# Kernel tuning notes

Measured on AMD Instinct MI355X. Metric: run time of the kernel, lower is better.

Reference implementation:

```python
import jax, jax.numpy as jnp
import numpy as np

EMBED_DIM = 512
NUM_HEADS = 16
WIN = (8, 8)
N_TOK = WIN[0] * WIN[1]           # 64 tokens per window
HEAD_DIM = EMBED_DIM // NUM_HEADS  # 32
SCALE = HEAD_DIM ** -0.5
B_WIN = 1024                       # batch * num_windows
NUM_WINDOWS = 256                  # windows per image -> batch images = 4


def _relative_bias_index(window_size):
    wh, ww = window_size
    coords = np.stack(np.meshgrid(np.arange(wh), np.arange(ww), indexing='ij'))  # (2, wh, ww)
    flat = coords.reshape(2, -1)                                   # (2, N)
    rel = (flat[:, :, None] - flat[:, None, :]).transpose(1, 2, 0)  # (N, N, 2)
    rel[:, :, 0] += wh - 1
    rel[:, :, 1] += ww - 1
    rel[:, :, 0] *= 2 * ww - 1
    return rel.sum(-1)  # (N, N) int


def setup_inputs() -> dict:
    key = jax.random.key(0)
    ks = jax.random.split(key, 6)
    x = jax.random.normal(ks[0], (B_WIN, N_TOK, EMBED_DIM), dtype=jnp.float32)
    attention_mask = jax.random.normal(ks[1], (NUM_WINDOWS, N_TOK, N_TOK), dtype=jnp.float32)
    qkv_w = jax.random.normal(ks[2], (EMBED_DIM, 3 * EMBED_DIM), dtype=jnp.float32) * 0.02
    qkv_b = jnp.zeros((3 * EMBED_DIM,), dtype=jnp.float32)
    proj_w = jax.random.normal(ks[3], (EMBED_DIM, EMBED_DIM), dtype=jnp.float32) * 0.02
    proj_b = jnp.zeros((EMBED_DIM,), dtype=jnp.float32)
    n_bias = (2 * WIN[0] - 1) * (2 * WIN[1] - 1)  # 225
    bias_table = jax.random.normal(ks[4], (n_bias, NUM_HEADS), dtype=jnp.float32) * 0.02
    rel_index = jnp.asarray(_relative_bias_index(WIN), dtype=jnp.int32)  # (N, N)
    return {"x": x, "attention_mask": attention_mask, "qkv_w": qkv_w, "qkv_b": qkv_b,
            "proj_w": proj_w, "proj_b": proj_b, "bias_table": bias_table, "rel_index": rel_index}


def reference(x, attention_mask, qkv_w, qkv_b, proj_w, proj_b, bias_table, rel_index):
    B, N, C = x.shape
    nw = attention_mask.shape[0]
    bimg = B // nw
    qkv = x @ qkv_w + qkv_b                              # (B, N, 3C)
    # original rearrange 'b n (h d c) -> d b n h c' groups last dim as (heads, 3, head_dim)
    qkv = qkv.reshape(B, N, NUM_HEADS, 3, HEAD_DIM)
    q, k, v = qkv[..., 0, :], qkv[..., 1, :], qkv[..., 2, :]  # each (B, N, H, hd)
    attn = jnp.einsum('bqhd,bkhd->bhqk', q, k) * SCALE        # (B, H, N, N)
    bias = bias_table[rel_index].transpose(2, 0, 1)           # (H, N, N)
    attn = attn + bias[None]
    attn = attn.reshape(bimg, nw, NUM_HEADS, N, N) + attention_mask[None, :, None]
    attn = jax.nn.softmax(attn, axis=-1).reshape(B, NUM_HEADS, N, N)
    out = jnp.einsum('bhqk,bkhd->bqhd', attn, v).reshape(B, N, C)
    return out @ proj_w + proj_b
```

## Files before the change

### kernel.cpp

```cpp
#include <hip/hip_runtime.h>
#include <hip/hip_bf16.h>


typedef unsigned short u16;
typedef __bf16 bx8 __attribute__((ext_vector_type(8)));
typedef float f4_t __attribute__((ext_vector_type(4)));

#define QKV_ELEMS 33554432ull
#define SCALE 0.17677669529663687f

static __device__ __forceinline__ u16 f2b(float f) {
    return __builtin_bit_cast(u16, (__bf16)f);
}

typedef const unsigned int __attribute__((address_space(1)))* gas_t;
typedef unsigned int __attribute__((address_space(3)))* las_t;
static __device__ __forceinline__ void glds16(const void* g, void* l) {
    __builtin_amdgcn_global_load_lds((gas_t)g, (las_t)l, 16, 0, 0);
}

__global__ __launch_bounds__(256) void prep_k(
    const float* __restrict__ X, u16* __restrict__ Xb,
    const float* __restrict__ qkv_w, u16* __restrict__ Wt1,
    const float* __restrict__ proj_w, u16* __restrict__ Wt2,
    const float* __restrict__ bias_t, const int* __restrict__ rel,
    float* __restrict__ biasf) {
    const int b = blockIdx.x;
    if (b < 16384) {
        size_t i = ((size_t)b * 256 + threadIdx.x) * 8;
        float4 v0 = *(const float4*)(X + i);
        float4 v1 = *(const float4*)(X + i + 4);
        ushort4 p0, p1;
        p0.x = f2b(v0.x); p0.y = f2b(v0.y); p0.z = f2b(v0.z); p0.w = f2b(v0.w);
        p1.x = f2b(v1.x); p1.y = f2b(v1.y); p1.z = f2b(v1.z); p1.w = f2b(v1.w);
        *(ushort4*)(Xb + i) = p0;
        *(ushort4*)(Xb + i + 4) = p1;
    } else if (b < 16384 + 3072) {
        int idx = (b - 16384) * 256 + threadIdx.x;
        int n = idx >> 9, k = idx & 511;
        Wt1[idx] = f2b(qkv_w[(size_t)k * 1536 + n]);
    } else if (b < 16384 + 4096) {
        int idx = (b - 16384 - 3072) * 256 + threadIdx.x;
        int n = idx >> 9, k = idx & 511;
        Wt2[idx] = f2b(proj_w[(size_t)k * 512 + n]);
    } else {
        int idx = (b - 16384 - 4096) * 256 + threadIdx.x;
        int h = idx >> 12, rc = idx & 4095;
        biasf[idx] = bias_t[rel[rc] * 16 + h];
    }
}


#define MF1(av, bv, mt, nt)                                                   \
    acc[mt][nt] = __builtin_amdgcn_mfma_f32_16x16x32_bf16(av, bv,             \
                                                          acc[mt][nt], 0, 0, 0);
#define MF4(av, mt, B)                                                        \
    MF1(av, B[0], mt, 0) MF1(av, B[1], mt, 1)                                 \
    MF1(av, B[2], mt, 2) MF1(av, B[3], mt, 3)

#define PH_EVEN(T, DOST, BCUR)                                                \
    {                                                                         \
        asm volatile("s_barrier" ::: "memory");                               \
        const char* aT = ldsA + ((T) & 3) * 16384 + wm * 8192 + foff;         \
        aHi[0] = *(const bx8*)(aT + 4096);                                    \
        aHi[1] = *(const bx8*)(aT + 5120);                                    \
        aHi[2] = *(const bx8*)(aT + 6144);                                    \
        aHi[3] = *(const bx8*)(aT + 7168);                                    \
        if (DOST) STAGE_A((T) + 3);                                           \
        asm volatile("s_waitcnt lgkmcnt(4)" ::: "memory");                    \
        __builtin_amdgcn_sched_barrier(0);                                    \
        __builtin_amdgcn_s_setprio(1);                                        \
        MF4(aLo[0], 0, BCUR) MF4(aLo[1], 1, BCUR)                             \
        MF4(aLo[2], 2, BCUR) MF4(aLo[3], 3, BCUR)                             \
        __builtin_amdgcn_s_setprio(0);                                        \
    }

#define PH_ODD(T, DOST, VMC, DORD, BCUR, BNXT)                                \
    {                                                                         \
        if ((VMC) == 6) asm volatile("s_waitcnt vmcnt(6)" ::: "memory");      \
        else if ((VMC) == 4) asm volatile("s_waitcnt vmcnt(4)" ::: "memory"); \
        else if ((VMC) == 0) asm volatile("s_waitcnt vmcnt(0)" ::: "memory"); \
        asm volatile("s_barrier" ::: "memory");                               \
        if (DORD) {                                                           \
            const char* aN = ldsA + (((T) + 1) & 3) * 16384 + wm * 8192 + foff;\
            const char* bN = ldsB + (((T) + 1) & 3) * 16384 + wn * 4096 + foff;\
            BNXT[0] = *(const bx8*)(bN);                                      \
            BNXT[1] = *(const bx8*)(bN + 1024);                               \
            BNXT[2] = *(const bx8*)(bN + 2048);                               \
            BNXT[3] = *(const bx8*)(bN + 3072);                               \
            aLo[0] = *(const bx8*)(aN);                                       \
            aLo[1] = *(const bx8*)(aN + 1024);                                \
            aLo[2] = *(const bx8*)(aN + 2048);                                \
            aLo[3] = *(const bx8*)(aN + 3072);                                \
        }                                                                     \
        if (DOST) STAGE_B((T) + 3);                                           \
        if (DORD) asm volatile("s_waitcnt lgkmcnt(8)" ::: "memory");          \
        else      asm volatile("s_waitcnt lgkmcnt(0)" ::: "memory");          \
        __builtin_amdgcn_sched_barrier(0);                                    \
        __builtin_amdgcn_s_setprio(1);                                        \
        MF4(aHi[0], 4, BCUR) MF4(aHi[1], 5, BCUR)                             \
        MF4(aHi[2], 6, BCUR) MF4(aHi[3], 7, BCUR)                             \
        __builtin_amdgcn_s_setprio(0);                                        \
    }

template <int MODE>
__global__ __launch_bounds__(512, 2) void gemm256_k(
    const u16* __restrict__ A, const u16* __restrict__ Bt,
    const float* __restrict__ bias, void* __restrict__ Out) {
    extern __shared__ __align__(16) char smem[];
    const int tid = threadIdx.x;
    const int wave = tid >> 6, lane = tid & 63;
    const int l16 = lane & 15, quad = lane >> 4;
    const int wm = wave >> 2, wn = wave & 3;

    const int NT_COL = (MODE == 0) ? 6 : 2;
    const int NWG = (MODE == 0) ? 1536 : 512;
    const int bid = blockIdx.x;
    const int swz = (bid & 7) * (NWG >> 3) + (bid >> 3);
    const int m0 = (swz / NT_COL) << 8;
    const int n0 = (swz % NT_COL) << 8;

    char* const ldsA = smem;
    char* const ldsB = smem + 65536;

    const int lr = lane >> 2, lc = lane & 3;
    const int swzc = (lc ^ ((lr >> 1) & 3)) * 8;
    const int stoff = wave * 1024;

    const u16* Asrc0;
    const u16* Asrc1;
    if (MODE == 0) {
        const int r0 = m0 + wave * 16 + lr;
        Asrc0 = A + (size_t)r0 * 512 + swzc;
        Asrc1 = Asrc0 + (size_t)128 * 512;
    } else {
        const int r0 = m0 + wave * 16 + lr, r1 = r0 + 128;
        Asrc0 = A + (size_t)(r0 >> 6) * 2048 + (r0 & 63) * 32 + swzc;
        Asrc1 = A + (size_t)(r1 >> 6) * 2048 + (r1 & 63) * 32 + swzc;
    }
    const u16* Bsrc0 = Bt + (size_t)(n0 + wave * 16 + lr) * 512 + swzc;
    const u16* Bsrc1 = Bsrc0 + (size_t)128 * 512;

    auto STAGE_A = [&](int T) {
        char* d = ldsA + (T & 3) * 16384 + stoff;
        if (MODE == 0) {
            glds16(Asrc0 + T * 32, d);
            glds16(Asrc1 + T * 32, d + 8192);
        } else {
            glds16(Asrc0 + (size_t)T * 2097152, d);
            glds16(Asrc1 + (size_t)T * 2097152, d + 8192);
        }
    };
    auto STAGE_B = [&](int T) {
        char* d = ldsB + (T & 3) * 16384 + stoff;
        glds16(Bsrc0 + T * 32, d);
        glds16(Bsrc1 + T * 32, d + 8192);
    };

    const int foff = l16 * 64 + ((quad ^ ((l16 >> 1) & 3)) * 16);

    f4_t acc[8][4];
#pragma unroll
    for (int i = 0; i < 8; ++i)
#pragma unroll
        for (int j = 0; j < 4; ++j) acc[i][j] = (f4_t){0.f, 0.f, 0.f, 0.f};

    bx8 aLo[4], aHi[4], bA[4], bB[4];

    STAGE_A(0); STAGE_B(0); STAGE_A(1); STAGE_B(1); STAGE_A(2); STAGE_B(2);
    asm volatile("s_waitcnt vmcnt(8)" ::: "memory");
    asm volatile("s_barrier" ::: "memory");
    {
        const char* aT = ldsA + wm * 8192 + foff;
        const char* bT = ldsB + wn * 4096 + foff;
        bA[0] = *(const bx8*)(bT);
        bA[1] = *(const bx8*)(bT + 1024);
        bA[2] = *(const bx8*)(bT + 2048);
        bA[3] = *(const bx8*)(bT + 3072);
        aLo[0] = *(const bx8*)(aT);
        aLo[1] = *(const bx8*)(aT + 1024);
        aLo[2] = *(const bx8*)(aT + 2048);
        aLo[3] = *(const bx8*)(aT + 3072);
    }

    PH_EVEN(0, 1, bA)  PH_ODD(0, 1, 6, 1, bA, bB)
    PH_EVEN(1, 1, bB)  PH_ODD(1, 1, 6, 1, bB, bA)
    PH_EVEN(2, 1, bA)  PH_ODD(2, 1, 6, 1, bA, bB)
    PH_EVEN(3, 1, bB)  PH_ODD(3, 1, 6, 1, bB, bA)
    PH_EVEN(4, 1, bA)  PH_ODD(4, 1, 6, 1, bA, bB)
    PH_EVEN(5, 1, bB)  PH_ODD(5, 1, 6, 1, bB, bA)
    PH_EVEN(6, 1, bA)  PH_ODD(6, 1, 6, 1, bA, bB)
    PH_EVEN(7, 1, bB)  PH_ODD(7, 1, 6, 1, bB, bA)
    PH_EVEN(8, 1, bA)  PH_ODD(8, 1, 6, 1, bA, bB)
    PH_EVEN(9, 1, bB)  PH_ODD(9, 1, 6, 1, bB, bA)
    PH_EVEN(10, 1, bA) PH_ODD(10, 1, 6, 1, bA, bB)
    PH_EVEN(11, 1, bB) PH_ODD(11, 1, 6, 1, bB, bA)
    PH_EVEN(12, 1, bA) PH_ODD(12, 1, 6, 1, bA, bB)
    PH_EVEN(13, 0, bB) PH_ODD(13, 0, 4, 1, bB, bA)
    PH_EVEN(14, 0, bA) PH_ODD(14, 0, 0, 1, bA, bB)
    PH_EVEN(15, 0, bB) PH_ODD(15, 0, -1, 0, bB, bA)

    __syncthreads();

    float bv[4];
#pragma unroll
    for (int nt = 0; nt < 4; ++nt) bv[nt] = bias[n0 + wn * 64 + nt * 16 + l16];

    if (MODE == 0) {
        u16* c_s = (u16*)smem;
        u16* qkvp = (u16*)Out;
        const int cg = n0 + wave * 32;
        const int hh = cg / 96;
        const int which = (cg - hh * 96) >> 5;
        u16* plane = qkvp + (size_t)which * QKV_ELEMS + (size_t)hh * 2048;
#pragma unroll
        for (int p = 0; p < 2; ++p) {
            if (wm == p) {
#pragma unroll
                for (int mt = 0; mt < 8; ++mt)
#pragma unroll
                    for (int nt = 0; nt < 4; ++nt)
#pragma unroll
                        for (int i = 0; i < 4; ++i)
                            c_s[(mt * 16 + quad * 4 + i) * 264 +
                                wn * 64 + nt * 16 + l16] =
                                f2b(acc[mt][nt][i] + bv[nt]);
            }
            __syncthreads();
#pragma unroll
            for (int j = 0; j < 8; ++j) {
                int row = j * 16 + (lane >> 2);
                int gm = m0 + p * 128 + row;
                int w_win = gm >> 6, tok = gm & 63;
                uint4 v = *(const uint4*)&c_s[row * 264 + wave * 32 +
                                              (lane & 3) * 8];
                *(uint4*)(plane + (size_t)w_win * 32768 + tok * 32 +
                          (lane & 3) * 8) = v;
            }
            __syncthreads();
        }
    } else {
        float* c_sf = (float*)smem;
        float* Of = (float*)Out;
#pragma unroll
        for (int p = 0; p < 4; ++p) {
            if (wm == (p >> 1)) {
                const int mtb = (p & 1) * 4;
#pragma unroll
                for (int mt2 = 0; mt2 < 4; ++mt2)
#pragma unroll
                    for (int nt = 0; nt < 4; ++nt)
#pragma unroll
                        for (int i = 0; i < 4; ++i)
                            c_sf[(mt2 * 16 + quad * 4 + i) * 264 +
                                 wn * 64 + nt * 16 + l16] =
                                acc[mtb + mt2][nt][i] + bv[nt];
            }
            __syncthreads();
#pragma unroll
            for (int j = 0; j < 8; ++j) {
                int flat = tid + 512 * j;
                int r = flat >> 6, c4 = (flat & 63) * 4;
                float4 v = *(const float4*)&c_sf[r * 264 + c4];
                *(float4*)&Of[(size_t)(m0 + p * 64 + r) * 512 + n0 + c4] = v;
            }
            __syncthreads();
        }
    }
}

__global__ __launch_bounds__(256, 4) void attn_k(
    const u16* __restrict__ qkv, const float* __restrict__ mask,
    const float* __restrict__ biasf, u16* __restrict__ attn_out) {
    const int bx = blockIdx.x;
    const int w = bx >> 4, h = bx & 15;
    const int wmk = w & 255;
    const int tid = threadIdx.x;
    const int wave = tid >> 6, lane = tid & 63;
    const int quad = lane >> 4, l16 = lane & 15;

    __shared__ alignas(16) u16 q_s[64 * 40];
    __shared__ alignas(16) u16 k_s[64 * 40];
    __shared__ alignas(16) u16 vT[32 * 72];
    __shared__ alignas(16) float s_s[64 * 65];
    __shared__ alignas(16) u16 p_s[64 * 72];

    const size_t base = (size_t)((w << 4) + h) * 2048;
    {
        int tok = tid >> 2, d0 = (tid & 3) * 8;
        uint4 qv = *(const uint4*)(qkv + base + tid * 8);
        *(uint4*)&q_s[tok * 40 + d0] = qv;
        uint4 kv = *(const uint4*)(qkv + QKV_ELEMS + base + tid * 8);
        *(uint4*)&k_s[tok * 40 + d0] = kv;
        uint4 vv = *(const uint4*)(qkv + 2 * QKV_ELEMS + base + tid * 8);
        const u16* pv = (const u16*)&vv;
#pragma unroll
        for (int j = 0; j < 8; ++j) vT[(d0 + j) * 72 + tok] = pv[j];
    }
    __syncthreads();

    {
        bx8 a = *(const bx8*)&q_s[(wave * 16 + l16) * 40 + quad * 8];
#pragma unroll
        for (int nt = 0; nt < 4; ++nt) {
            bx8 b = *(const bx8*)&k_s[(nt * 16 + l16) * 40 + quad * 8];
            f4_t acc = (f4_t){0.f, 0.f, 0.f, 0.f};
            acc = __builtin_amdgcn_mfma_f32_16x16x32_bf16(a, b, acc, 0, 0, 0);
#pragma unroll
            for (int i = 0; i < 4; ++i) {
                int r = wave * 16 + quad * 4 + i;
                int c = nt * 16 + l16;
                float s = acc[i] * SCALE + biasf[(h << 12) + (r << 6) + c] +
                          mask[((size_t)wmk * 64 + r) * 64 + c];
                s_s[r * 65 + c] = s;
            }
        }
    }
    __syncthreads();

    {
        int row = tid >> 2, j = (tid & 3) * 16;
        float mx = -1e30f;
#pragma unroll
        for (int cc = 0; cc < 16; ++cc) mx = fmaxf(mx, s_s[row * 65 + j + cc]);
        mx = fmaxf(mx, __shfl_xor(mx, 1));
        mx = fmaxf(mx, __shfl_xor(mx, 2));
        float e[16], sum = 0.f;
#pragma unroll
        for (int cc = 0; cc < 16; ++cc) {
            e[cc] = __expf(s_s[row * 65 + j + cc] - mx);
            sum += e[cc];
        }
        sum += __shfl_xor(sum, 1);
        sum += __shfl_xor(sum, 2);
        float inv = 1.f / sum;
#pragma unroll
        for (int cc = 0; cc < 16; ++cc) p_s[row * 72 + j + cc] = f2b(e[cc] * inv);
    }
    __syncthreads();

    {
        u16* os = (u16*)s_s;
#pragma unroll
        for (int nt = 0; nt < 2; ++nt) {
            f4_t acc = (f4_t){0.f, 0.f, 0.f, 0.f};
#pragma unroll
            for (int ks = 0; ks < 2; ++ks) {
                bx8 a = *(const bx8*)&p_s[(wave * 16 + l16) * 72 + ks * 32 + quad * 8];
                bx8 b = *(const bx8*)&vT[(nt * 16 + l16) * 72 + ks * 32 + quad * 8];
                acc = __builtin_amdgcn_mfma_f32_16x16x32_bf16(a, b, acc, 0, 0, 0);
            }
#pragma unroll
            for (int i = 0; i < 4; ++i)
                os[(wave * 16 + quad * 4 + i) * 40 + nt * 16 + l16] =
                    f2b(acc[i]);
        }
        __syncthreads();
        int tok = tid >> 2, d8 = (tid & 3) * 8;
        uint4 v = *(const uint4*)&os[tok * 40 + d8];
        *(uint4*)(attn_out + ((((size_t)h << 10) + w) << 11) + tid * 8) = v;
    }
}

extern "C" void kernel_launch(void* const* d_in, const int* in_sizes, int n_in,
                              void* d_out, int out_size, void* d_ws,
                              size_t ws_size, hipStream_t stream) {
    const float* x      = (const float*)d_in[0];
    const float* mask   = (const float*)d_in[1];
    const float* qkv_w  = (const float*)d_in[2];
    const float* qkv_b  = (const float*)d_in[3];
    const float* proj_w = (const float*)d_in[4];
    const float* proj_b = (const float*)d_in[5];
    const float* bias_t = (const float*)d_in[6];
    const int*   rel    = (const int*)d_in[7];
    float* out = (float*)d_out;

    char* ws = (char*)d_ws;
    u16* Wt1 = (u16*)ws;      ws += (size_t)1536 * 512 * 2;
    u16* Wt2 = (u16*)ws;      ws += (size_t)512 * 512 * 2;
    float* biasf = (float*)ws; ws += (size_t)16 * 64 * 64 * 4;
    u16* qkv = (u16*)ws;      ws += 3 * QKV_ELEMS * 2;
    u16* attn = (u16*)ws;     ws += QKV_ELEMS * 2;
    u16* xb = attn;

    prep_k<<<20736, 256, 0, stream>>>(x, xb, qkv_w, Wt1, proj_w, Wt2,
                                      bias_t, rel, biasf);
    gemm256_k<0><<<1536, 512, 131072, stream>>>(xb, Wt1, qkv_b, qkv);
    attn_k<<<16384, 256, 0, stream>>>(qkv, mask, biasf, attn);
    gemm256_k<1><<<512, 512, 131072, stream>>>(attn, Wt2, proj_b, out);
}
```

Measured before the change: 484.9 us.

## Restructure GEMM main loop to K=64 tiles with double buffering

The GEMM kernel's mainloop moves from sixteen K=32 steps over a 4-stage LDS ring to eight K=64 steps with two LDS buffers of 64KB each. The LDS swizzle and staging layout change to match. This halves the number of barriers and lets each stage issue larger batches of async loads. The cost is a shallower prefetch depth (one tile ahead, with a full vmcnt(0) wait before each barrier), which can expose global-load latency.

```diff
diff --git a/kernel.cpp b/kernel.cpp
--- a/kernel.cpp
+++ b/kernel.cpp
@@ -51,60 +51,75 @@
 }
 
 
-#define MF1(av, bv, mt, nt)                                                   \
-    acc[mt][nt] = __builtin_amdgcn_mfma_f32_16x16x32_bf16(av, bv,             \
-                                                          acc[mt][nt], 0, 0, 0);
-#define MF4(av, mt, B)                                                        \
-    MF1(av, B[0], mt, 0) MF1(av, B[1], mt, 1)                                 \
-    MF1(av, B[2], mt, 2) MF1(av, B[3], mt, 3)
-
-#define PH_EVEN(T, DOST, BCUR)                                                \
+#define MF1(av, bv, mi, nt)                                                   \
+    acc[mi][nt] = __builtin_amdgcn_mfma_f32_16x16x32_bf16(av, bv,             \
+                                                          acc[mi][nt], 0, 0, 0);
+#define MF16(A4, mb, B4)                                                      \
+    MF1(A4[0], B4[0], (mb)+0, 0) MF1(A4[0], B4[1], (mb)+0, 1)                 \
+    MF1(A4[0], B4[2], (mb)+0, 2) MF1(A4[0], B4[3], (mb)+0, 3)                 \
+    MF1(A4[1], B4[0], (mb)+1, 0) MF1(A4[1], B4[1], (mb)+1, 1)                 \
+    MF1(A4[1], B4[2], (mb)+1, 2) MF1(A4[1], B4[3], (mb)+1, 3)                 \
+    MF1(A4[2], B4[0], (mb)+2, 0) MF1(A4[2], B4[1], (mb)+2, 1)                 \
+    MF1(A4[2], B4[2], (mb)+2, 2) MF1(A4[2], B4[3], (mb)+2, 3)                 \
+    MF1(A4[3], B4[0], (mb)+3, 0) MF1(A4[3], B4[1], (mb)+3, 1)                 \
+    MF1(A4[3], B4[2], (mb)+3, 2) MF1(A4[3], B4[3], (mb)+3, 3)
+
+#define ARD4(dst, sb, mh, kh)                                                 \
+    dst[0] = *(const bx8*)((sb) + awoff + ((mh)*4+0)*2048 + aoffk##kh);       \
+    dst[1] = *(const bx8*)((sb) + awoff + ((mh)*4+1)*2048 + aoffk##kh);       \
+    dst[2] = *(const bx8*)((sb) + awoff + ((mh)*4+2)*2048 + aoffk##kh);       \
+    dst[3] = *(const bx8*)((sb) + awoff + ((mh)*4+3)*2048 + aoffk##kh);
+#define BRD4(dst, sb, kh)                                                     \
+    dst[0] = *(const bx8*)((sb) + bwoff + 0*2048 + aoffk##kh);                \
+    dst[1] = *(const bx8*)((sb) + bwoff + 1*2048 + aoffk##kh);                \
+    dst[2] = *(const bx8*)((sb) + bwoff + 2*2048 + aoffk##kh);                \
+    dst[3] = *(const bx8*)((sb) + bwoff + 3*2048 + aoffk##kh);
+
+#define TILE64(T, DOST, LAST)                                                 \
     {                                                                         \
-        asm volatile("s_barrier" ::: "memory");                               \
-        const char* aT = ldsA + ((T) & 3) * 16384 + wm * 8192 + foff;         \
-        aHi[0] = *(const bx8*)(aT + 4096);                                    \
-        aHi[1] = *(const bx8*)(aT + 5120);                                    \
-        aHi[2] = *(const bx8*)(aT + 6144);                                    \
-        aHi[3] = *(const bx8*)(aT + 7168);                                    \
-        if (DOST) STAGE_A((T) + 3);                                           \
+        const char* sb = smem + ((T) & 1) * 65536;                            \
+        const char* sn = smem + (((T) + 1) & 1) * 65536;                      \
+                          \
+        ARD4(aN, sb, 1, 0)                                                    \
+        if (DOST) STAGE((T) + 1);                                             \
         asm volatile("s_waitcnt lgkmcnt(4)" ::: "memory");                    \
         __builtin_amdgcn_sched_barrier(0);                                    \
         __builtin_amdgcn_s_setprio(1);                                        \
-        MF4(aLo[0], 0, BCUR) MF4(aLo[1], 1, BCUR)                             \
-        MF4(aLo[2], 2, BCUR) MF4(aLo[3], 3, BCUR)                             \
+        MF16(aC, 0, b0)                                                       \
         __builtin_amdgcn_s_setprio(0);                                        \
-    }
-
-#define PH_ODD(T, DOST, VMC, DORD, BCUR, BNXT)                                \
-    {                                                                         \
-        if ((VMC) == 6) asm volatile("s_waitcnt vmcnt(6)" ::: "memory");      \
-        else if ((VMC) == 4) asm volatile("s_waitcnt vmcnt(4)" ::: "memory"); \
-        else if ((VMC) == 0) asm volatile("s_waitcnt vmcnt(0)" ::: "memory"); \
-        asm volatile("s_barrier" ::: "memory");                               \
-        if (DORD) {                                                           \
-            const char* aN = ldsA + (((T) + 1) & 3) * 16384 + wm * 8192 + foff;\
-            const char* bN = ldsB + (((T) + 1) & 3) * 16384 + wn * 4096 + foff;\
-            BNXT[0] = *(const bx8*)(bN);                                      \
-            BNXT[1] = *(const bx8*)(bN + 1024);                               \
-            BNXT[2] = *(const bx8*)(bN + 2048);                               \
-            BNXT[3] = *(const bx8*)(bN + 3072);                               \
-            aLo[0] = *(const bx8*)(aN);                                       \
-            aLo[1] = *(const bx8*)(aN + 1024);                                \
-            aLo[2] = *(const bx8*)(aN + 2048);                                \
-            aLo[3] = *(const bx8*)(aN + 3072);                                \
-        }                                                                     \
-        if (DOST) STAGE_B((T) + 3);                                           \
-        if (DORD) asm volatile("s_waitcnt lgkmcnt(8)" ::: "memory");          \
-        else      asm volatile("s_waitcnt lgkmcnt(0)" ::: "memory");          \
+                               \
+        ARD4(aC, sb, 0, 1)                                                    \
+        BRD4(b1, sb, 1)                                                       \
+        asm volatile("s_waitcnt lgkmcnt(8)" ::: "memory");                    \
         __builtin_amdgcn_sched_barrier(0);                                    \
         __builtin_amdgcn_s_setprio(1);                                        \
-        MF4(aHi[0], 4, BCUR) MF4(aHi[1], 5, BCUR)                             \
-        MF4(aHi[2], 6, BCUR) MF4(aHi[3], 7, BCUR)                             \
+        MF16(aN, 4, b0)                                                       \
         __builtin_amdgcn_s_setprio(0);                                        \
+                                     \
+        ARD4(aN, sb, 1, 1)                                                    \
+        asm volatile("s_waitcnt lgkmcnt(4)" ::: "memory");                    \
+        __builtin_amdgcn_sched_barrier(0);                                    \
+        __builtin_amdgcn_s_setprio(1);                                        \
+        MF16(aC, 0, b1)                                                       \
+        __builtin_amdgcn_s_setprio(0);                                        \
+         \
+        if (!(LAST)) {                                                        \
+            asm volatile("s_waitcnt vmcnt(0)" ::: "memory");                  \
+            asm volatile("s_barrier" ::: "memory");                           \
+            ARD4(aC, sn, 0, 0)                                                \
+            BRD4(b0, sn, 0)                                                   \
+            asm volatile("s_waitcnt lgkmcnt(8)" ::: "memory");                \
+        } else {                                                              \
+            asm volatile("s_waitcnt lgkmcnt(0)" ::: "memory");                \
+        }                                                                     \
+        __builtin_amdgcn_sched_barrier(0);                                    \
+        __builtin_amdgcn_s_setprio(1);                                        \
+        MF16(aN, 4, b1)                                                       \
+        __builtin_amdgcn_s_setprio(0);                                        \
     }
 
 template <int MODE>
-__global__ __launch_bounds__(512, 2) void gemm256_k(
+__global__ __launch_bounds__(512, 2) void gemm64_k(
     const u16* __restrict__ A, const u16* __restrict__ Bt,
     const float* __restrict__ bias, void* __restrict__ Out) {
     extern __shared__ __align__(16) char smem[];
@@ -120,44 +135,45 @@
     const int m0 = (swz / NT_COL) << 8;
     const int n0 = (swz % NT_COL) << 8;
 
-    char* const ldsA = smem;
-    char* const ldsB = smem + 65536;
-
-    const int lr = lane >> 2, lc = lane & 3;
-    const int swzc = (lc ^ ((lr >> 1) & 3)) * 8;
+    const int sc = (lane & 7) ^ (lane >> 3);
     const int stoff = wave * 1024;
 
-    const u16* Asrc0;
-    const u16* Asrc1;
+    const u16* Abase;
+    size_t aplaneSel = 0, aoff1[4];
     if (MODE == 0) {
-        const int r0 = m0 + wave * 16 + lr;
-        Asrc0 = A + (size_t)r0 * 512 + swzc;
-        Asrc1 = Asrc0 + (size_t)128 * 512;
+        Abase = A + (size_t)(m0 + 8 * wave + (lane >> 3)) * 512 + sc * 8;
     } else {
-        const int r0 = m0 + wave * 16 + lr, r1 = r0 + 128;
-        Asrc0 = A + (size_t)(r0 >> 6) * 2048 + (r0 & 63) * 32 + swzc;
-        Asrc1 = A + (size_t)(r1 >> 6) * 2048 + (r1 & 63) * 32 + swzc;
-    }
-    const u16* Bsrc0 = Bt + (size_t)(n0 + wave * 16 + lr) * 512 + swzc;
-    const u16* Bsrc1 = Bsrc0 + (size_t)128 * 512;
-
-    auto STAGE_A = [&](int T) {
-        char* d = ldsA + (T & 3) * 16384 + stoff;
+        aplaneSel = (size_t)(sc >> 2) * 2097152;
+#pragma unroll
+        for (int ci = 0; ci < 4; ++ci)
+            aoff1[ci] = (size_t)((m0 >> 6) + ci) * 2048 +
+                        (8 * wave + (lane >> 3)) * 32 + (sc & 3) * 8;
+    }
+    const u16* Bbase = Bt + (size_t)(n0 + 8 * wave + (lane >> 3)) * 512 + sc * 8;
+
+    auto STAGE = [&](int T) {
+        char* sb = smem + (T & 1) * 65536;
         if (MODE == 0) {
-            glds16(Asrc0 + T * 32, d);
-            glds16(Asrc1 + T * 32, d + 8192);
+            const u16* a = Abase + (size_t)T * 64;
+#pragma unroll
+            for (int ci = 0; ci < 4; ++ci)
+                glds16(a + (size_t)ci * 32768, sb + ci * 8192 + stoff);
         } else {
-            glds16(Asrc0 + (size_t)T * 2097152, d);
-            glds16(Asrc1 + (size_t)T * 2097152, d + 8192);
-        }
+            const u16* a = A + (size_t)(2 * T) * 2097152 + aplaneSel;
+#pragma unroll
+            for (int ci = 0; ci < 4; ++ci)
+                glds16(a + aoff1[ci], sb + ci * 8192 + stoff);
+        }
+        const u16* bs = Bbase + (size_t)T * 64;
+#pragma unroll
+        for (int ci = 0; ci < 4; ++ci)
+            glds16(bs + (size_t)ci * 32768, sb + 32768 + ci * 8192 + stoff);
     };
-    auto STAGE_B = [&](int T) {
-        char* d = ldsB + (T & 3) * 16384 + stoff;
-        glds16(Bsrc0 + T * 32, d);
-        glds16(Bsrc1 + T * 32, d + 8192);
-    };
-
-    const int foff = l16 * 64 + ((quad ^ ((l16 >> 1) & 3)) * 16);
+
+    const int awoff = wm * 16384;
+    const int bwoff = 32768 + wn * 8192;
+    const int aoffk0 = l16 * 128 + (((0 * 4 + quad) ^ (l16 & 7)) * 16);
+    const int aoffk1 = l16 * 128 + (((1 * 4 + quad) ^ (l16 & 7)) * 16);
 
     f4_t acc[8][4];
 #pragma unroll
@@ -165,40 +181,25 @@
 #pragma unroll
         for (int j = 0; j < 4; ++j) acc[i][j] = (f4_t){0.f, 0.f, 0.f, 0.f};
 
-    bx8 aLo[4], aHi[4], bA[4], bB[4];
-
-    STAGE_A(0); STAGE_B(0); STAGE_A(1); STAGE_B(1); STAGE_A(2); STAGE_B(2);
-    asm volatile("s_waitcnt vmcnt(8)" ::: "memory");
+    bx8 aC[4], aN[4], b0[4], b1[4];
+
+    STAGE(0);
+    asm volatile("s_waitcnt vmcnt(0)" ::: "memory");
     asm volatile("s_barrier" ::: "memory");
     {
-        const char* aT = ldsA + wm * 8192 + foff;
-        const char* bT = ldsB + wn * 4096 + foff;
-        bA[0] = *(const bx8*)(bT);
-        bA[1] = *(const bx8*)(bT + 1024);
-        bA[2] = *(const bx8*)(bT + 2048);
-        bA[3] = *(const bx8*)(bT + 3072);
-        aLo[0] = *(const bx8*)(aT);
-        aLo[1] = *(const bx8*)(aT + 1024);
-        aLo[2] = *(const bx8*)(aT + 2048);
-        aLo[3] = *(const bx8*)(aT + 3072);
-    }
-
-    PH_EVEN(0, 1, bA)  PH_ODD(0, 1, 6, 1, bA, bB)
-    PH_EVEN(1, 1, bB)  PH_ODD(1, 1, 6, 1, bB, bA)
-    PH_EVEN(2, 1, bA)  PH_ODD(2, 1, 6, 1, bA, bB)
-    PH_EVEN(3, 1, bB)  PH_ODD(3, 1, 6, 1, bB, bA)
-    PH_EVEN(4, 1, bA)  PH_ODD(4, 1, 6, 1, bA, bB)
-    PH_EVEN(5, 1, bB)  PH_ODD(5, 1, 6, 1, bB, bA)
-    PH_EVEN(6, 1, bA)  PH_ODD(6, 1, 6, 1, bA, bB)
-    PH_EVEN(7, 1, bB)  PH_ODD(7, 1, 6, 1, bB, bA)
-    PH_EVEN(8, 1, bA)  PH_ODD(8, 1, 6, 1, bA, bB)
-    PH_EVEN(9, 1, bB)  PH_ODD(9, 1, 6, 1, bB, bA)
-    PH_EVEN(10, 1, bA) PH_ODD(10, 1, 6, 1, bA, bB)
-    PH_EVEN(11, 1, bB) PH_ODD(11, 1, 6, 1, bB, bA)
-    PH_EVEN(12, 1, bA) PH_ODD(12, 1, 6, 1, bA, bB)
-    PH_EVEN(13, 0, bB) PH_ODD(13, 0, 4, 1, bB, bA)
-    PH_EVEN(14, 0, bA) PH_ODD(14, 0, 0, 1, bA, bB)
-    PH_EVEN(15, 0, bB) PH_ODD(15, 0, -1, 0, bB, bA)
+        const char* sb = smem;
+        ARD4(aC, sb, 0, 0)
+        BRD4(b0, sb, 0)
+    }
+
+    TILE64(0, 1, 0)
+    TILE64(1, 1, 0)
+    TILE64(2, 1, 0)
+    TILE64(3, 1, 0)
+    TILE64(4, 1, 0)
+    TILE64(5, 1, 0)
+    TILE64(6, 1, 0)
+    TILE64(7, 0, 1)
 
     __syncthreads();
 
@@ -385,7 +386,7 @@
 
     prep_k<<<20736, 256, 0, stream>>>(x, xb, qkv_w, Wt1, proj_w, Wt2,
                                       bias_t, rel, biasf);
-    gemm256_k<0><<<1536, 512, 131072, stream>>>(xb, Wt1, qkv_b, qkv);
+    gemm64_k<0><<<1536, 512, 131072, stream>>>(xb, Wt1, qkv_b, qkv);
     attn_k<<<16384, 256, 0, stream>>>(qkv, mask, biasf, attn);
-    gemm256_k<1><<<512, 512, 131072, stream>>>(attn, Wt2, proj_b, out);
-}
+    gemm64_k<1><<<512, 512, 131072, stream>>>(attn, Wt2, proj_b, out);
+}
```

Result: no change. 482.9 us (-0.4%).
